# Performance work log

Hardware: AMD Instinct MI355X
Metric: run time of the kernel (lower is better)

Reference implementation:

```python
import jax, jax.numpy as jnp
import numpy as np

N_NODES = 100000
N_EDGES = 1000000
D_IN = 64
D_OUT = 64


def setup_inputs() -> dict:
    key = jax.random.key(0)
    k1, k2, k3, k4 = jax.random.split(key, 4)
    x = jax.random.normal(k1, (N_NODES, D_IN), dtype=jnp.float32)
    edge_index = jax.random.randint(k2, (2, N_EDGES), 0, N_NODES, dtype=jnp.int64)
    edge_weight = jax.random.uniform(k3, (N_EDGES,), dtype=jnp.float32)
    W = jax.random.normal(k4, (D_OUT, D_IN), dtype=jnp.float32) * (1.0 / np.sqrt(D_IN))
    bias = jnp.zeros((D_OUT,), dtype=jnp.float32)
    return {"x": x, "edge_index": edge_index, "edge_weight": edge_weight, "W": W, "bias": bias}


def reference(x, edge_index, edge_weight, W, bias):
    n = x.shape[0]
    self_loops = jnp.arange(n)
    row = jnp.concatenate([edge_index[0], self_loops])  # [E+N]
    col = jnp.concatenate([edge_index[1], self_loops])  # [E+N]
    ew = jnp.concatenate([edge_weight, jnp.ones((n,), x.dtype)])  # [E+N]
    # degree via scatter-add of edge weights into row nodes
    deg = jax.ops.segment_sum(ew, row, num_segments=n)  # [N]
    deg_safe = jnp.where(deg > 0, deg, 1.0)
    deg_inv_sqrt = jnp.where(deg > 0, jax.lax.rsqrt(deg_safe), 0.0)  # inf -> 0
    norm = deg_inv_sqrt[row] * ew * deg_inv_sqrt[col]  # [E+N]
    # gather-scale-scatter aggregation
    msg = x[col] * norm[:, None]  # [E+N, D_IN]
    out = jax.ops.segment_sum(msg, row, num_segments=n)  # [N, D_IN]
    return out @ W.T + bias
```

## Files before the change

kernel.cpp:

```cpp
#include <hip/hip_runtime.h>
#include <hip/hip_bf16.h>

#define D 64
#define K 24
#define M44 ((1ULL << 44) - 1)
#define SPILLCAP 65536

typedef __attribute__((ext_vector_type(4))) _Float16 half4;
typedef __attribute__((ext_vector_type(8))) _Float16 half8;

__global__ __launch_bounds__(256) void k_build(const int* __restrict__ rowi,
                                               const int* __restrict__ coli,
                                               const float* __restrict__ ew,
                                               unsigned long long* __restrict__ packed,
                                               unsigned int* __restrict__ slots,
                                               int4* __restrict__ spill,
                                               int* __restrict__ spillCnt, int nE,
                                               int prepBlocks,
                                               const float4* __restrict__ x4,
                                               half8* __restrict__ xh8, int nv) {
    int b = blockIdx.x;
    if (b < prepBlocks) {
        int t = b * 256 + threadIdx.x;
        if (t >= nv) return;
        float4 a = x4[2 * t], bb = x4[2 * t + 1];
        half8 h;
        h[0] = (_Float16)a.x; h[1] = (_Float16)a.y; h[2] = (_Float16)a.z; h[3] = (_Float16)a.w;
        h[4] = (_Float16)bb.x; h[5] = (_Float16)bb.y; h[6] = (_Float16)bb.z; h[7] = (_Float16)bb.w;
        xh8[t] = h;
        return;
    }
    int bp = b - prepBlocks;
    int p = bp & 7;
    int e = (bp >> 3) * 256 + threadIdx.x;
    if (e >= nE) return;
    int r = rowi[e];
    if ((r & 7) != p) return;
    int c = coli[e];
    float w = ew[e];
    unsigned long long fx = (unsigned long long)((double)w * 4294967296.0);
    unsigned long long old = atomicAdd(&packed[r], (1ULL << 44) | fx);
    int rank = (int)(old >> 44);
    if (rank < K) {
        int q = (int)(w * 32768.0f + 0.5f);
        if (q > 32767) q = 32767;
        slots[r * K + rank] = ((unsigned int)c << 15) | (unsigned int)q;
    } else {
        int pI = atomicAdd(spillCnt, 1);
        if (pI < SPILLCAP) spill[pI] = make_int4(r, c, __float_as_int(w), 0);
    }
}

__device__ __forceinline__ float dis_of(unsigned long long pk) {
    return rsqrtf(1.0f + (float)(pk & M44) * (1.0f / 4294967296.0f));
}

template <bool H>
__global__ __launch_bounds__(256) void k_gather_gemm(const float* __restrict__ x,
                                                     const _Float16* __restrict__ xh,
                                                     const unsigned long long* __restrict__ packed,
                                                     const unsigned int* __restrict__ slots,
                                                     const int4* __restrict__ spill,
                                                     const int* __restrict__ spillCnt,
                                                     const float* __restrict__ W,
                                                     const float* __restrict__ bias,
                                                     float* __restrict__ out, int n) {
    __shared__ float Bs[D * D];
    __shared__ float Ast[16 * D];
    float4* Ast4 = (float4*)Ast;
    int tid = threadIdx.x;

    const float4* W4 = (const float4*)W;
#pragma unroll
    for (int v = 0; v < 4; ++v) {
        int idx = tid + v * 256;
        int o  = idx >> 4;
        int kc = idx & 15;
        float4 wv = W4[idx];
        int gq = o >> 2, oo = o & 3;
        int cpos = 4 * ((gq + kc) & 15) + oo;
        Bs[(4 * kc + 0) * 64 + cpos] = wv.x;
        Bs[(4 * kc + 1) * 64 + cpos] = wv.y;
        Bs[(4 * kc + 2) * 64 + cpos] = wv.z;
        Bs[(4 * kc + 3) * 64 + cpos] = wv.w;
    }

    int j   = tid & 15;
    int grp = tid >> 4;
    int i0  = blockIdx.x * 16;
    int i   = i0 + grp;

    float4 acc = make_float4(0.f, 0.f, 0.f, 0.f);
    const float4* x4 = (const float4*)x;
    const half4*  xh4 = (const half4*)xh;
    if (i < n) {
        unsigned long long pk = packed[i];
        half4 hi; float4 xi;
        if constexpr (H) hi = xh4[i * 16 + j]; else xi = x4[i * 16 + j];
        int rawc = (int)(pk >> 44);
        int c_n = rawc < K ? rawc : K;
        int s = i * K;
        for (int off = 0; off < c_n; off += 16) {
            int idx = off + j;
            unsigned int rec = 0u;
            float wj = 0.f;
            if (idx < c_n) {
                rec = slots[s + idx];
                wj = (float)(rec & 32767u) * (1.0f / 32768.0f) * dis_of(packed[rec >> 15]);
            }
#pragma unroll
            for (int t = 0; t < 16; ++t) {
                int col = (int)((unsigned int)__shfl((int)rec, t, 16) >> 15);
                float w = __shfl(wj, t, 16);
                if constexpr (H) {
                    half4 hv = xh4[col * 16 + j];
                    acc.x += w * (float)hv[0]; acc.y += w * (float)hv[1];
                    acc.z += w * (float)hv[2]; acc.w += w * (float)hv[3];
                } else {
                    float4 xv = x4[col * 16 + j];
                    acc.x += w * xv.x; acc.y += w * xv.y;
                    acc.z += w * xv.z; acc.w += w * xv.w;
                }
            }
        }
        if (rawc > K) {
            int total = *spillCnt;
            if (total > SPILLCAP) total = SPILLCAP;
            for (int sp = 0; sp < total; ++sp) {
                int4 v = spill[sp];
                if (v.x == i) {
                    float w = __int_as_float(v.z) * dis_of(packed[v.y]);
                    if constexpr (H) {
                        half4 hv = xh4[v.y * 16 + j];
                        acc.x += w * (float)hv[0]; acc.y += w * (float)hv[1];
                        acc.z += w * (float)hv[2]; acc.w += w * (float)hv[3];
                    } else {
                        float4 xv = x4[v.y * 16 + j];
                        acc.x += w * xv.x; acc.y += w * xv.y;
                        acc.z += w * xv.z; acc.w += w * xv.w;
                    }
                }
            }
        }
        float di = dis_of(pk);
        if constexpr (H) {
            acc.x = di * (di * (float)hi[0] + acc.x);
            acc.y = di * (di * (float)hi[1] + acc.y);
            acc.z = di * (di * (float)hi[2] + acc.z);
            acc.w = di * (di * (float)hi[3] + acc.w);
        } else {
            acc.x = di * (di * xi.x + acc.x);
            acc.y = di * (di * xi.y + acc.y);
            acc.z = di * (di * xi.z + acc.z);
            acc.w = di * (di * xi.w + acc.w);
        }
    }
    Ast4[grp * 16 + ((j + (grp >> 2)) & 15)] = acc;
    __syncthreads();

    int row = tid >> 4;
    int cg  = tid & 15;
    float4 oacc = ((const float4*)bias)[cg];
#pragma unroll 4
    for (int kc = 0; kc < 16; ++kc) {
        float4 a4 = Ast4[row * 16 + ((kc + (row >> 2)) & 15)];
        int cp = 4 * ((cg + kc) & 15);
        float4 b0 = *(const float4*)&Bs[(4 * kc + 0) * 64 + cp];
        float4 b1 = *(const float4*)&Bs[(4 * kc + 1) * 64 + cp];
        float4 b2 = *(const float4*)&Bs[(4 * kc + 2) * 64 + cp];
        float4 b3 = *(const float4*)&Bs[(4 * kc + 3) * 64 + cp];
        oacc.x += a4.x * b0.x + a4.y * b1.x + a4.z * b2.x + a4.w * b3.x;
        oacc.y += a4.x * b0.y + a4.y * b1.y + a4.z * b2.y + a4.w * b3.y;
        oacc.z += a4.x * b0.z + a4.y * b1.z + a4.z * b2.z + a4.w * b3.z;
        oacc.w += a4.x * b0.w + a4.y * b1.w + a4.z * b2.w + a4.w * b3.w;
    }
    int r = i0 + row;
    if (r < n) ((float4*)out)[r * 16 + cg] = oacc;
}

extern "C" void kernel_launch(void* const* d_in, const int* in_sizes, int n_in,
                              void* d_out, int out_size, void* d_ws, size_t ws_size,
                              hipStream_t stream) {
    const float* x    = (const float*)d_in[0];
    const int*   ei   = (const int*)d_in[1];
    const float* ew   = (const float*)d_in[2];
    const float* W    = (const float*)d_in[3];
    const float* bias = (const float*)d_in[4];
    float* out = (float*)d_out;

    int n  = in_sizes[0] / D;
    int nE = in_sizes[2];
    const int* rowi = ei;
    const int* coli = ei + nE;

    char* w = (char*)d_ws;
    unsigned long long* packed = (unsigned long long*)w; w += (size_t)n * 8;
    int* spillCnt = (int*)w;                             w += 64;
    unsigned int* slots = (unsigned int*)w;              w += (size_t)n * K * 4;
    int4* spill = (int4*)w;                              w += (size_t)SPILLCAP * 16;
    _Float16* xh = (_Float16*)w;

    size_t need = (size_t)n * 8 + 64 + (size_t)n * K * 4 + (size_t)SPILLCAP * 16
                + (size_t)n * D * 2;
    int useH = ws_size >= need ? 1 : 0;

    int gE = (nE + 255) / 256;
    int buildBlocks = gE * 8;
    int nv = n * D / 8;
    int prepBlocks = useH ? (nv + 255) / 256 : 0;
    int gT = (n + 15) / 16;

    hipMemsetAsync(packed, 0, (size_t)n * 8 + 64, stream);
    k_build<<<prepBlocks + buildBlocks, 256, 0, stream>>>(
        rowi, coli, ew, packed, slots, spill, spillCnt, nE,
        prepBlocks, (const float4*)x, (half8*)xh, nv);
    if (useH)
        k_gather_gemm<true><<<gT, 256, 0, stream>>>(x, xh, packed, slots, spill, spillCnt, W, bias, out, n);
    else
        k_gather_gemm<false><<<gT, 256, 0, stream>>>(x, xh, packed, slots, spill, spillCnt, W, bias, out, n);
}
```

Baseline: 176.0 us.

## Prescale fp16 features by inverse sqrt degree and interleave node-to-block mapping

Adds a separate kernel that multiplies the fp16 copy of x by each node's inverse sqrt degree once. The gather then no longer has to do a dependent random load of packed[col] per edge to compute the source normalization, and the self-loop term drops one multiply. It also remaps blocks so each block handles nodes with a stride of 8, with the prep block count rounded up to a multiple of 8, apparently to spread work across XCDs or caches. The cost is an extra kernel launch plus a read and write pass over the fp16 x buffer, and the fp16 values are rounded once more after scaling.

Result: no change. 178.6 us (+1.5%).

```diff
diff --git a/kernel.cpp b/kernel.cpp
--- a/kernel.cpp
+++ b/kernel.cpp
@@ -55,6 +55,17 @@
     return rsqrtf(1.0f + (float)(pk & M44) * (1.0f / 4294967296.0f));
 }
 
+__global__ __launch_bounds__(256) void k_scale(const unsigned long long* __restrict__ packed,
+                                               half8* __restrict__ xh8, int nv8) {
+    int t = blockIdx.x * 256 + threadIdx.x;
+    if (t >= nv8) return;
+    float dis = dis_of(packed[t >> 3]);
+    half8 h = xh8[t];
+#pragma unroll
+    for (int k = 0; k < 8; ++k) h[k] = (_Float16)((float)h[k] * dis);
+    xh8[t] = h;
+}
+
 template <bool H>
 __global__ __launch_bounds__(256) void k_gather_gemm(const float* __restrict__ x,
                                                      const _Float16* __restrict__ xh,
@@ -87,8 +98,9 @@
 
     int j   = tid & 15;
     int grp = tid >> 4;
-    int i0  = blockIdx.x * 16;
-    int i   = i0 + grp;
+    int cls = blockIdx.x & 7;
+    int q   = blockIdx.x >> 3;
+    int i   = ((q * 16 + grp) << 3) + cls;
 
     float4 acc = make_float4(0.f, 0.f, 0.f, 0.f);
     const float4* x4 = (const float4*)x;
@@ -106,17 +118,20 @@
             float wj = 0.f;
             if (idx < c_n) {
                 rec = slots[s + idx];
-                wj = (float)(rec & 32767u) * (1.0f / 32768.0f) * dis_of(packed[rec >> 15]);
+                if constexpr (!H)
+                    wj = (float)(rec & 32767u) * (1.0f / 32768.0f) * dis_of(packed[rec >> 15]);
             }
 #pragma unroll
             for (int t = 0; t < 16; ++t) {
-                int col = (int)((unsigned int)__shfl((int)rec, t, 16) >> 15);
-                float w = __shfl(wj, t, 16);
+                unsigned int rt = (unsigned int)__shfl((int)rec, t, 16);
+                int col = (int)(rt >> 15);
                 if constexpr (H) {
+                    float w = (float)(rt & 32767u) * (1.0f / 32768.0f);
                     half4 hv = xh4[col * 16 + j];
                     acc.x += w * (float)hv[0]; acc.y += w * (float)hv[1];
                     acc.z += w * (float)hv[2]; acc.w += w * (float)hv[3];
                 } else {
+                    float w = __shfl(wj, t, 16);
                     float4 xv = x4[col * 16 + j];
                     acc.x += w * xv.x; acc.y += w * xv.y;
                     acc.z += w * xv.z; acc.w += w * xv.w;
@@ -129,12 +144,13 @@
             for (int sp = 0; sp < total; ++sp) {
                 int4 v = spill[sp];
                 if (v.x == i) {
-                    float w = __int_as_float(v.z) * dis_of(packed[v.y]);
                     if constexpr (H) {
+                        float w = __int_as_float(v.z);
                         half4 hv = xh4[v.y * 16 + j];
                         acc.x += w * (float)hv[0]; acc.y += w * (float)hv[1];
                         acc.z += w * (float)hv[2]; acc.w += w * (float)hv[3];
                     } else {
+                        float w = __int_as_float(v.z) * dis_of(packed[v.y]);
                         float4 xv = x4[v.y * 16 + j];
                         acc.x += w * xv.x; acc.y += w * xv.y;
                         acc.z += w * xv.z; acc.w += w * xv.w;
@@ -144,10 +160,10 @@
         }
         float di = dis_of(pk);
         if constexpr (H) {
-            acc.x = di * (di * (float)hi[0] + acc.x);
-            acc.y = di * (di * (float)hi[1] + acc.y);
-            acc.z = di * (di * (float)hi[2] + acc.z);
-            acc.w = di * (di * (float)hi[3] + acc.w);
+            acc.x = di * ((float)hi[0] + acc.x);
+            acc.y = di * ((float)hi[1] + acc.y);
+            acc.z = di * ((float)hi[2] + acc.z);
+            acc.w = di * ((float)hi[3] + acc.w);
         } else {
             acc.x = di * (di * xi.x + acc.x);
             acc.y = di * (di * xi.y + acc.y);
@@ -174,7 +190,7 @@
         oacc.z += a4.x * b0.z + a4.y * b1.z + a4.z * b2.z + a4.w * b3.z;
         oacc.w += a4.x * b0.w + a4.y * b1.w + a4.z * b2.w + a4.w * b3.w;
     }
-    int r = i0 + row;
+    int r = ((q * 16 + row) << 3) + cls;
     if (r < n) ((float4*)out)[r * 16 + cg] = oacc;
 }
 
@@ -207,15 +223,19 @@
     int gE = (nE + 255) / 256;
     int buildBlocks = gE * 8;
     int nv = n * D / 8;
-    int prepBlocks = useH ? (nv + 255) / 256 : 0;
-    int gT = (n + 15) / 16;
+    int prepBlocks = useH ? ((((nv + 255) / 256) + 7) & ~7) : 0;
+    int nPerClass = (n + 7) / 8;
+    int gT = 8 * ((nPerClass + 15) / 16);
 
     hipMemsetAsync(packed, 0, (size_t)n * 8 + 64, stream);
     k_build<<<prepBlocks + buildBlocks, 256, 0, stream>>>(
         rowi, coli, ew, packed, slots, spill, spillCnt, nE,
         prepBlocks, (const float4*)x, (half8*)xh, nv);
-    if (useH)
+    if (useH) {
+        int nv8 = n * 8;
+        k_scale<<<(nv8 + 255) / 256, 256, 0, stream>>>(packed, (half8*)xh, nv8);
         k_gather_gemm<true><<<gT, 256, 0, stream>>>(x, xh, packed, slots, spill, spillCnt, W, bias, out, n);
-    else
+    } else {
         k_gather_gemm<false><<<gT, 256, 0, stream>>>(x, xh, packed, slots, spill, spillCnt, W, bias, out, n);
-}
+    }
+}
```
